# Kernel tuning notes

Measured on AMD Instinct MI355X. Metric: run time of the kernel, lower is better.

The kernel has to match this reference:

```python
import jax, jax.numpy as jnp
import numpy as np

PI = 3.141592653589793
MARGIN = 9.0


def setup_inputs() -> dict:
    key = jax.random.key(0)
    k1, k2, k3, k4 = jax.random.split(key, 4)
    num_nodes, dim = 100000, 512
    num_edges, num_rel = 1000000, 64
    node_embeddings = jax.random.normal(k1, (num_nodes, dim), dtype=jnp.float32)
    edge_index = jax.random.randint(k2, (2, num_edges), 0, num_nodes, dtype=jnp.int64)
    relation_type = jax.random.randint(k3, (num_edges,), 0, num_rel, dtype=jnp.int64)
    # nn.init.uniform_(-0.1, 0.1)
    relation_emb = jax.random.uniform(k4, (num_rel, dim // 2), dtype=jnp.float32,
                                      minval=-0.1, maxval=0.1)
    temperature = jnp.ones((), dtype=jnp.float32)
    bias = jnp.ones((), dtype=jnp.float32)
    return {"node_embeddings": node_embeddings, "edge_index": edge_index,
            "relation_type": relation_type, "relation_emb": relation_emb,
            "temperature": temperature, "bias": bias}


def reference(node_embeddings, edge_index, relation_type, relation_emb, temperature, bias):
    # gather head/tail node embeddings: [num_edges, dim]
    head = node_embeddings[edge_index[0]]
    tail = node_embeddings[edge_index[1]]
    # relation phase lookup: [num_edges, dim//2]
    phase_rel = relation_emb[relation_type] / (MARGIN / PI)
    half = node_embeddings.shape[1] // 2
    re_head, im_head = head[:, :half], head[:, half:]
    re_tail, im_tail = tail[:, :half], tail[:, half:]
    re_rel = jnp.cos(phase_rel)
    im_rel = jnp.sin(phase_rel)
    # complex rotation: (re_head + i*im_head) * (re_rel + i*im_rel)
    re_diff = re_head * re_rel - im_head * im_rel - re_tail
    im_diff = re_head * im_rel + im_head * re_rel - im_tail
    distance = jnp.sqrt(re_diff * re_diff + im_diff * im_diff).mean(axis=-1)
    return -(distance / temperature) + bias
```

## Files before the change

### kernel.cpp

```cpp
#include <hip/hip_runtime.h>
#include <math.h>

#define PHASE_K  0.3490658503988659f

__device__ __forceinline__ void tiny_sincos(float x, float* s, float* c) {
    float t = x * x;
    *s = x * fmaf(t, -1.0f / 6.0f, 1.0f);
    *c = fmaf(t, fmaf(t, 1.0f / 24.0f, -0.5f), 1.0f);
}

__device__ __forceinline__ unsigned int f2bf_rne(float f) {
    unsigned int u = __float_as_uint(f);
    return (u + 0x7FFFu + ((u >> 16) & 1u)) >> 16;
}

__global__ __launch_bounds__(256) void build_rot_kernel(
    const float* __restrict__ rel_emb, unsigned int* __restrict__ rot, int n)
{
    int i = blockIdx.x * 256 + threadIdx.x;
    if (i >= n) return;
    float s, c;
    tiny_sincos(rel_emb[i] * PHASE_K, &s, &c);
    rot[i] = (f2bf_rne(s) << 16) | f2bf_rne(c);
}

__global__ __launch_bounds__(256) void convert_kernel(
    const float* __restrict__ node, unsigned int* __restrict__ tbl, int nnodes)
{
    int p = blockIdx.x * 256 + threadIdx.x;
    if (p >= nnodes * 64) return;
    int n = p >> 6, q = p & 63;
    const float4 re = *(const float4*)(node + (size_t)n * 512 + 4 * q);
    const float4 im = *(const float4*)(node + (size_t)n * 512 + 256 + 4 * q);
    uint4 w;
    w.x = f2bf_rne(re.x) | (f2bf_rne(im.x) << 16);
    w.y = f2bf_rne(re.y) | (f2bf_rne(im.y) << 16);
    w.z = f2bf_rne(re.z) | (f2bf_rne(im.z) << 16);
    w.w = f2bf_rne(re.w) | (f2bf_rne(im.w) << 16);
    *(uint4*)(tbl + (size_t)n * 256 + 4 * q) = w;
}

__device__ __forceinline__ float dim_term(unsigned int hw, unsigned int tw,
                                          unsigned int rw) {
    float rh = __uint_as_float(hw << 16);
    float ih = __uint_as_float(hw & 0xFFFF0000u);
    float rt = __uint_as_float(tw << 16);
    float it = __uint_as_float(tw & 0xFFFF0000u);
    float c  = __uint_as_float(rw << 16);
    float s  = __uint_as_float(rw & 0xFFFF0000u);
    float rd = fmaf(rh, c, -fmaf(ih, s, rt));
    float id = fmaf(rh, s,  fmaf(ih, c, -it));
    return __builtin_amdgcn_sqrtf(fmaf(rd, rd, id * id));
}

template <int CTRL>
__device__ __forceinline__ float dpp_shr_add(float x) {
    int y = __builtin_amdgcn_update_dpp(0, __float_as_int(x), CTRL, 0xF, 0xF, true);
    return x + __int_as_float(y);
}

__global__ __launch_bounds__(256) void rotate_score_v3(
    const unsigned int* __restrict__ tbl,
    const unsigned int* __restrict__ rot,
    const int*   __restrict__ eidx,
    const int*   __restrict__ rel,
    const float* __restrict__ temp,
    const float* __restrict__ bias,
    float*       __restrict__ out,
    int nedges)
{
    int gtid = blockIdx.x * 256 + threadIdx.x;
    int edge = gtid >> 4;
    int sub  = threadIdx.x & 15;
    if (edge >= nedges) return;

    int h = eidx[edge];
    int t = eidx[nedges + edge];
    int r = rel[edge];

    const unsigned int* ph = tbl + (size_t)h * 256 + 4 * sub;
    const unsigned int* pt = tbl + (size_t)t * 256 + 4 * sub;
    const unsigned int* pr = rot + (r << 8) + 4 * sub;

    uint4 h0 = *(const uint4*)(ph);
    uint4 h1 = *(const uint4*)(ph + 64);
    uint4 h2 = *(const uint4*)(ph + 128);
    uint4 h3 = *(const uint4*)(ph + 192);
    uint4 t0 = *(const uint4*)(pt);
    uint4 t1 = *(const uint4*)(pt + 64);
    uint4 t2 = *(const uint4*)(pt + 128);
    uint4 t3 = *(const uint4*)(pt + 192);
    uint4 r0 = *(const uint4*)(pr);
    uint4 r1 = *(const uint4*)(pr + 64);
    uint4 r2 = *(const uint4*)(pr + 128);
    uint4 r3 = *(const uint4*)(pr + 192);

    float sum = 0.0f;
    sum += dim_term(h0.x, t0.x, r0.x);
    sum += dim_term(h0.y, t0.y, r0.y);
    sum += dim_term(h0.z, t0.z, r0.z);
    sum += dim_term(h0.w, t0.w, r0.w);
    sum += dim_term(h1.x, t1.x, r1.x);
    sum += dim_term(h1.y, t1.y, r1.y);
    sum += dim_term(h1.z, t1.z, r1.z);
    sum += dim_term(h1.w, t1.w, r1.w);
    sum += dim_term(h2.x, t2.x, r2.x);
    sum += dim_term(h2.y, t2.y, r2.y);
    sum += dim_term(h2.z, t2.z, r2.z);
    sum += dim_term(h2.w, t2.w, r2.w);
    sum += dim_term(h3.x, t3.x, r3.x);
    sum += dim_term(h3.y, t3.y, r3.y);
    sum += dim_term(h3.z, t3.z, r3.z);
    sum += dim_term(h3.w, t3.w, r3.w);

    sum = dpp_shr_add<0x111>(sum);
    sum = dpp_shr_add<0x112>(sum);
    sum = dpp_shr_add<0x114>(sum);
    sum = dpp_shr_add<0x118>(sum);

    if (sub == 15)
        out[edge] = bias[0] - (sum * (1.0f / 256.0f)) / temp[0];
}

__global__ __launch_bounds__(256) void rotate_score_fp32(
    const float* __restrict__ node, const int* __restrict__ eidx,
    const int* __restrict__ rel, const float* __restrict__ rel_emb,
    const float* __restrict__ temp, const float* __restrict__ bias,
    float* __restrict__ out, int nedges)
{
    int gtid = blockIdx.x * 256 + threadIdx.x;
    int edge = gtid >> 6;
    int lane = threadIdx.x & 63;
    if (edge >= nedges) return;

    int e_u = __builtin_amdgcn_readfirstlane(edge);
    int h = __builtin_amdgcn_readfirstlane(eidx[e_u]);
    int t = __builtin_amdgcn_readfirstlane(eidx[nedges + e_u]);
    int r = __builtin_amdgcn_readfirstlane(rel[e_u]);
    int d = lane << 2;

    const float4* ph = (const float4*)(node + (size_t)h * 512 + d);
    const float4* pt = (const float4*)(node + (size_t)t * 512 + d);
    float4 rh = ph[0], ih = ph[64], rt = pt[0], it = pt[64];
    float4 pe = *(const float4*)(rel_emb + (r << 8) + d);

    float cx, sx, cy, sy, cz, sz, cw, sw;
    tiny_sincos(pe.x * PHASE_K, &sx, &cx);
    tiny_sincos(pe.y * PHASE_K, &sy, &cy);
    tiny_sincos(pe.z * PHASE_K, &sz, &cz);
    tiny_sincos(pe.w * PHASE_K, &sw, &cw);

    float sum, rd, id;
    rd = fmaf(rh.x, cx, -fmaf(ih.x, sx, rt.x));
    id = fmaf(rh.x, sx,  fmaf(ih.x, cx, -it.x));
    sum  = __builtin_amdgcn_sqrtf(fmaf(rd, rd, id * id));
    rd = fmaf(rh.y, cy, -fmaf(ih.y, sy, rt.y));
    id = fmaf(rh.y, sy,  fmaf(ih.y, cy, -it.y));
    sum += __builtin_amdgcn_sqrtf(fmaf(rd, rd, id * id));
    rd = fmaf(rh.z, cz, -fmaf(ih.z, sz, rt.z));
    id = fmaf(rh.z, sz,  fmaf(ih.z, cz, -it.z));
    sum += __builtin_amdgcn_sqrtf(fmaf(rd, rd, id * id));
    rd = fmaf(rh.w, cw, -fmaf(ih.w, sw, rt.w));
    id = fmaf(rh.w, sw,  fmaf(ih.w, cw, -it.w));
    sum += __builtin_amdgcn_sqrtf(fmaf(rd, rd, id * id));

    #pragma unroll
    for (int m = 1; m < 64; m <<= 1)
        sum += __shfl_xor(sum, m);

    if (lane == 0)
        out[edge] = bias[0] - (sum * (1.0f / 256.0f)) / temp[0];
}

extern "C" void kernel_launch(void* const* d_in, const int* in_sizes, int n_in,
                              void* d_out, int out_size, void* d_ws, size_t ws_size,
                              hipStream_t stream) {
    const float* node    = (const float*)d_in[0];
    const int*   eidx    = (const int*)  d_in[1];
    const int*   rel     = (const int*)  d_in[2];
    const float* rel_emb = (const float*)d_in[3];
    const float* temp    = (const float*)d_in[4];
    const float* bias    = (const float*)d_in[5];
    float*       out     = (float*)d_out;

    int nedges = in_sizes[1] / 2;
    int nnodes = in_sizes[0] / 512;
    int nrot   = in_sizes[3];

    size_t tbl_bytes = (size_t)nnodes * 1024;
    size_t need      = tbl_bytes + (size_t)nrot * 4;

    if (ws_size >= need) {
        unsigned int* tbl = (unsigned int*)d_ws;
        unsigned int* rot = (unsigned int*)((char*)d_ws + tbl_bytes);

        build_rot_kernel<<<(nrot + 255) / 256, 256, 0, stream>>>(rel_emb, rot, nrot);

        int cblocks = (nnodes * 64 + 255) / 256;
        convert_kernel<<<cblocks, 256, 0, stream>>>(node, tbl, nnodes);

        int gblocks = (nedges * 16 + 255) / 256;
        rotate_score_v3<<<gblocks, 256, 0, stream>>>(
            tbl, rot, eidx, rel, temp, bias, out, nedges);
    } else {
        int eblocks = (nedges + 3) / 4;
        rotate_score_fp32<<<eblocks, 256, 0, stream>>>(
            node, eidx, rel, rel_emb, temp, bias, out, nedges);
    }
}
```

Before: 556.4 us.

## Quantize node table to 12-bit per-row scaled ints to cut gather bytes

Replaces the bf16 packed node table with a 12-bit fixed-point encoding that uses a per-node max-abs scale, shrinking each row from 1024 to 768 bytes plus a 4-byte scale. The scoring kernel gathers the smaller rows, unpacks them with bit manipulation and dequantizes with an FMA. The aim is to reduce gather memory traffic in the bandwidth-bound scoring pass, at the cost of extra ALU unpacking work, a cross-lane max reduction in the convert pass, and lower precision than bf16 for rows with outliers.

```diff
diff --git a/kernel.cpp b/kernel.cpp
--- a/kernel.cpp
+++ b/kernel.cpp
@@ -24,28 +24,57 @@
     rot[i] = (f2bf_rne(s) << 16) | f2bf_rne(c);
 }
 
-__global__ __launch_bounds__(256) void convert_kernel(
-    const float* __restrict__ node, unsigned int* __restrict__ tbl, int nnodes)
-{
-    int p = blockIdx.x * 256 + threadIdx.x;
-    if (p >= nnodes * 64) return;
-    int n = p >> 6, q = p & 63;
-    const float4 re = *(const float4*)(node + (size_t)n * 512 + 4 * q);
-    const float4 im = *(const float4*)(node + (size_t)n * 512 + 256 + 4 * q);
-    uint4 w;
-    w.x = f2bf_rne(re.x) | (f2bf_rne(im.x) << 16);
-    w.y = f2bf_rne(re.y) | (f2bf_rne(im.y) << 16);
-    w.z = f2bf_rne(re.z) | (f2bf_rne(im.z) << 16);
-    w.w = f2bf_rne(re.w) | (f2bf_rne(im.w) << 16);
-    *(uint4*)(tbl + (size_t)n * 256 + 4 * q) = w;
-}
-
-__device__ __forceinline__ float dim_term(unsigned int hw, unsigned int tw,
-                                          unsigned int rw) {
-    float rh = __uint_as_float(hw << 16);
-    float ih = __uint_as_float(hw & 0xFFFF0000u);
-    float rt = __uint_as_float(tw << 16);
-    float it = __uint_as_float(tw & 0xFFFF0000u);
+__global__ __launch_bounds__(256) void convert12_kernel(
+    const float* __restrict__ node, unsigned int* __restrict__ tbl,
+    float* __restrict__ scl, int nnodes)
+{
+    int wid  = (blockIdx.x * 256 + threadIdx.x) >> 6;
+    int lane = threadIdx.x & 63;
+    if (wid >= nnodes) return;
+
+    const float* row = node + (size_t)wid * 512;
+    float4 re = *(const float4*)(row + 4 * lane);
+    float4 im = *(const float4*)(row + 256 + 4 * lane);
+
+    float m = fmaxf(fmaxf(fabsf(re.x), fabsf(re.y)), fmaxf(fabsf(re.z), fabsf(re.w)));
+    m = fmaxf(m, fmaxf(fmaxf(fabsf(im.x), fabsf(im.y)), fmaxf(fabsf(im.z), fabsf(im.w))));
+    #pragma unroll
+    for (int k = 1; k < 64; k <<= 1) m = fmaxf(m, __shfl_xor(m, k));
+    m = fmaxf(m, 1e-20f);
+    float inv = 2047.0f / m;
+
+    float rv[4] = {re.x, re.y, re.z, re.w};
+    float iv[4] = {im.x, im.y, im.z, im.w};
+    unsigned int ur[4], ui[4];
+    #pragma unroll
+    for (int j = 0; j < 4; ++j) {
+        ur[j] = (unsigned int)((int)rintf(rv[j] * inv) + 2048);
+        ui[j] = (unsigned int)((int)rintf(iv[j] * inv) + 2048);
+    }
+    unsigned int B[12];
+    #pragma unroll
+    for (int j = 0; j < 4; ++j) {
+        B[3*j]   = (ur[j] >> 4) & 0xFFu;
+        B[3*j+1] = (ui[j] >> 4) & 0xFFu;
+        B[3*j+2] = (ur[j] & 0xFu) | ((ui[j] & 0xFu) << 4);
+    }
+    unsigned int w0 = B[0] | (B[1] << 8) | (B[2]  << 16) | (B[3]  << 24);
+    unsigned int w1 = B[4] | (B[5] << 8) | (B[6]  << 16) | (B[7]  << 24);
+    unsigned int w2 = B[8] | (B[9] << 8) | (B[10] << 16) | (B[11] << 24);
+
+    unsigned int* dst = tbl + (size_t)wid * 192 + 3 * lane;
+    dst[0] = w0; dst[1] = w1; dst[2] = w2;
+    if (lane == 0) scl[wid] = m * (1.0f / 2047.0f);
+}
+
+__device__ __forceinline__ float dim_term12(
+    unsigned int uhr, unsigned int uhi, unsigned int utr, unsigned int uti,
+    unsigned int rw, float sh, float oh, float st, float ot)
+{
+    float rh = fmaf((float)uhr, sh, oh);
+    float ih = fmaf((float)uhi, sh, oh);
+    float rt = fmaf((float)utr, st, ot);
+    float it = fmaf((float)uti, st, ot);
     float c  = __uint_as_float(rw << 16);
     float s  = __uint_as_float(rw & 0xFFFF0000u);
     float rd = fmaf(rh, c, -fmaf(ih, s, rt));
@@ -53,14 +82,44 @@
     return __builtin_amdgcn_sqrtf(fmaf(rd, rd, id * id));
 }
 
+__device__ __forceinline__ float group_terms(
+    unsigned int hw0, unsigned int hw1, unsigned int hw2,
+    unsigned int tw0, unsigned int tw1, unsigned int tw2,
+    uint4 R, float sh, float oh, float st, float ot)
+{
+    float acc;
+    acc  = dim_term12(((hw0 & 255u) << 4) | ((hw0 >> 16) & 15u),
+                      (((hw0 >> 8) & 255u) << 4) | ((hw0 >> 20) & 15u),
+                      ((tw0 & 255u) << 4) | ((tw0 >> 16) & 15u),
+                      (((tw0 >> 8) & 255u) << 4) | ((tw0 >> 20) & 15u),
+                      R.x, sh, oh, st, ot);
+    acc += dim_term12(((hw0 >> 24) << 4) | ((hw1 >> 8) & 15u),
+                      ((hw1 & 255u) << 4) | ((hw1 >> 12) & 15u),
+                      ((tw0 >> 24) << 4) | ((tw1 >> 8) & 15u),
+                      ((tw1 & 255u) << 4) | ((tw1 >> 12) & 15u),
+                      R.y, sh, oh, st, ot);
+    acc += dim_term12((((hw1 >> 16) & 255u) << 4) | (hw2 & 15u),
+                      ((hw1 >> 24) << 4) | ((hw2 >> 4) & 15u),
+                      (((tw1 >> 16) & 255u) << 4) | (tw2 & 15u),
+                      ((tw1 >> 24) << 4) | ((tw2 >> 4) & 15u),
+                      R.z, sh, oh, st, ot);
+    acc += dim_term12((((hw2 >> 8) & 255u) << 4) | ((hw2 >> 24) & 15u),
+                      (((hw2 >> 16) & 255u) << 4) | (hw2 >> 28),
+                      (((tw2 >> 8) & 255u) << 4) | ((tw2 >> 24) & 15u),
+                      (((tw2 >> 16) & 255u) << 4) | (tw2 >> 28),
+                      R.w, sh, oh, st, ot);
+    return acc;
+}
+
 template <int CTRL>
 __device__ __forceinline__ float dpp_shr_add(float x) {
     int y = __builtin_amdgcn_update_dpp(0, __float_as_int(x), CTRL, 0xF, 0xF, true);
     return x + __int_as_float(y);
 }
 
-__global__ __launch_bounds__(256) void rotate_score_v3(
+__global__ __launch_bounds__(256) void rotate_score_v4(
     const unsigned int* __restrict__ tbl,
+    const float*        __restrict__ scl,
     const unsigned int* __restrict__ rot,
     const int*   __restrict__ eidx,
     const int*   __restrict__ rel,
@@ -78,40 +137,21 @@
     int t = eidx[nedges + edge];
     int r = rel[edge];
 
-    const unsigned int* ph = tbl + (size_t)h * 256 + 4 * sub;
-    const unsigned int* pt = tbl + (size_t)t * 256 + 4 * sub;
-    const unsigned int* pr = rot + (r << 8) + 4 * sub;
-
-    uint4 h0 = *(const uint4*)(ph);
-    uint4 h1 = *(const uint4*)(ph + 64);
-    uint4 h2 = *(const uint4*)(ph + 128);
-    uint4 h3 = *(const uint4*)(ph + 192);
-    uint4 t0 = *(const uint4*)(pt);
-    uint4 t1 = *(const uint4*)(pt + 64);
-    uint4 t2 = *(const uint4*)(pt + 128);
-    uint4 t3 = *(const uint4*)(pt + 192);
-    uint4 r0 = *(const uint4*)(pr);
-    uint4 r1 = *(const uint4*)(pr + 64);
-    uint4 r2 = *(const uint4*)(pr + 128);
-    uint4 r3 = *(const uint4*)(pr + 192);
-
-    float sum = 0.0f;
-    sum += dim_term(h0.x, t0.x, r0.x);
-    sum += dim_term(h0.y, t0.y, r0.y);
-    sum += dim_term(h0.z, t0.z, r0.z);
-    sum += dim_term(h0.w, t0.w, r0.w);
-    sum += dim_term(h1.x, t1.x, r1.x);
-    sum += dim_term(h1.y, t1.y, r1.y);
-    sum += dim_term(h1.z, t1.z, r1.z);
-    sum += dim_term(h1.w, t1.w, r1.w);
-    sum += dim_term(h2.x, t2.x, r2.x);
-    sum += dim_term(h2.y, t2.y, r2.y);
-    sum += dim_term(h2.z, t2.z, r2.z);
-    sum += dim_term(h2.w, t2.w, r2.w);
-    sum += dim_term(h3.x, t3.x, r3.x);
-    sum += dim_term(h3.y, t3.y, r3.y);
-    sum += dim_term(h3.z, t3.z, r3.z);
-    sum += dim_term(h3.w, t3.w, r3.w);
+    const uint4* ph = (const uint4*)(tbl + (size_t)h * 192 + 12 * sub);
+    const uint4* pt = (const uint4*)(tbl + (size_t)t * 192 + 12 * sub);
+    const uint4* pr = (const uint4*)(rot + (r << 8) + 16 * sub);
+
+    uint4 H0 = ph[0], H1 = ph[1], H2 = ph[2];
+    uint4 T0 = pt[0], T1 = pt[1], T2 = pt[2];
+    uint4 R0 = pr[0], R1 = pr[1], R2 = pr[2], R3 = pr[3];
+    float sh = scl[h], st = scl[t];
+    float oh = -2048.0f * sh, ot = -2048.0f * st;
+
+    float sum;
+    sum  = group_terms(H0.x, H0.y, H0.z,  T0.x, T0.y, T0.z,  R0, sh, oh, st, ot);
+    sum += group_terms(H0.w, H1.x, H1.y,  T0.w, T1.x, T1.y,  R1, sh, oh, st, ot);
+    sum += group_terms(H1.z, H1.w, H2.x,  T1.z, T1.w, T2.x,  R2, sh, oh, st, ot);
+    sum += group_terms(H2.y, H2.z, H2.w,  T2.y, T2.z, T2.w,  R3, sh, oh, st, ot);
 
     sum = dpp_shr_add<0x111>(sum);
     sum = dpp_shr_add<0x112>(sum);
@@ -187,21 +227,23 @@
     int nnodes = in_sizes[0] / 512;
     int nrot   = in_sizes[3];
 
-    size_t tbl_bytes = (size_t)nnodes * 1024;
-    size_t need      = tbl_bytes + (size_t)nrot * 4;
+    size_t tbl_bytes = (size_t)nnodes * 768;
+    size_t scl_bytes = (size_t)nnodes * 4;
+    size_t need      = tbl_bytes + scl_bytes + (size_t)nrot * 4;
 
     if (ws_size >= need) {
         unsigned int* tbl = (unsigned int*)d_ws;
-        unsigned int* rot = (unsigned int*)((char*)d_ws + tbl_bytes);
+        float*        scl = (float*)((char*)d_ws + tbl_bytes);
+        unsigned int* rot = (unsigned int*)((char*)d_ws + tbl_bytes + scl_bytes);
 
         build_rot_kernel<<<(nrot + 255) / 256, 256, 0, stream>>>(rel_emb, rot, nrot);
 
         int cblocks = (nnodes * 64 + 255) / 256;
-        convert_kernel<<<cblocks, 256, 0, stream>>>(node, tbl, nnodes);
+        convert12_kernel<<<cblocks, 256, 0, stream>>>(node, tbl, scl, nnodes);
 
         int gblocks = (nedges * 16 + 255) / 256;
-        rotate_score_v3<<<gblocks, 256, 0, stream>>>(
-            tbl, rot, eidx, rel, temp, bias, out, nedges);
+        rotate_score_v4<<<gblocks, 256, 0, stream>>>(
+            tbl, scl, rot, eidx, rel, temp, bias, out, nedges);
     } else {
         int eblocks = (nedges + 3) / 4;
         rotate_score_fp32<<<eblocks, 256, 0, stream>>>(
```

Measured after the change: 544.1 us. -2.2%, faster.
